# Kernel tuning notes

Measured on AMD Instinct MI355X. Metric: run time of the kernel, lower is better.

The kernel has to match this reference:

```python
import jax, jax.numpy as jnp
import numpy as np

G = 16       # groups
GRID = 25    # hardcoded self.grid
EPS = 1e-5   # BatchNorm eps


def _gconv(x, w, pad):
    # x: (B, Cin, H, W), w: (Cout, Cin//G, kh, kw); grouped conv, stride 1
    return jax.lax.conv_general_dilated(
        x, w, window_strides=(1, 1), padding=[(pad, pad), (pad, pad)],
        feature_group_count=G)


def _bn_relu(h, g, b, m, v):
    # h: (G, B, C, H, W); per-group-instance BN params: (G, C). Inference BN.
    scale = (g / jnp.sqrt(v + EPS))[:, None, :, None, None]
    return jax.nn.relu((h - m[:, None, :, None, None]) * scale + b[:, None, :, None, None])


def setup_inputs() -> dict:
    key = jax.random.key(0)
    ks = jax.random.split(key, 11)
    B, C, H, W = 2, 256, 24, 24
    AC = GRID * C  # 6400 affinity channels
    return {
        "x":  jax.random.normal(ks[0], (B, C, H, W), jnp.float32),
        "W1": jax.random.normal(ks[1], (G, C, C // G, 3, 3), jnp.float32) * 0.05,
        "g1": jax.random.uniform(ks[2], (G, C), jnp.float32, 0.5, 1.5),
        "b1": jax.random.normal(ks[3], (G, C), jnp.float32) * 0.1,
        "m1": jax.random.normal(ks[4], (G, C), jnp.float32) * 0.1,
        "v1": jax.random.uniform(ks[5], (G, C), jnp.float32, 0.5, 1.5),
        "W2": jax.random.normal(ks[6], (G, AC, C // G, 1, 1), jnp.float32) * 0.05,
        "g2": jax.random.uniform(ks[7], (G, AC), jnp.float32, 0.5, 1.5),
        "b2": jax.random.normal(ks[8], (G, AC), jnp.float32) * 0.1,
        "m2": jax.random.normal(ks[9], (G, AC), jnp.float32) * 0.1,
        "v2": jax.random.uniform(ks[10], (G, AC), jnp.float32, 0.5, 1.5),
    }


def reference(x, W1, g1, b1, m1, v1, W2, g2, b2, m2, v2):
    B, C, H, W = x.shape
    Cg = C // G
    # 16 independent grouped 3x3 convs over the same input, batched via vmap
    h1 = jax.vmap(lambda w: _gconv(x, w, 1))(W1)          # (G, B, C, H, W)
    h1 = _bn_relu(h1, g1, b1, m1, v1)
    # grouped 1x1 conv with padding=1 (faithful to source -> spatial grows to H+2, W+2)
    a = jax.vmap(lambda h, w: _gconv(h, w, 1))(h1, W2)    # (G, B, 25C, H+2, W+2)
    a = _bn_relu(a, g2, b2, m2, v2)
    pooled = a.mean(axis=(-2, -1))                        # adaptive avg pool -> (G, B, 25C)
    xv = pooled.reshape(G, B, G, GRID * Cg)               # (G, B, G, 25*Cg)
    aff = jnp.einsum('ibkm,iblm->ibkl', xv, xv)           # (G, B, G, G) = theta @ phi
    idx = jnp.arange(G)
    aff_i = aff[idx, :, idx, :] / G                       # aff[:, i], /N  -> (G, B, G)
    ex = h1.reshape(G, B, G, Cg * H * W)
    # torch.matmul((B,G), (B,G,M)) broadcasts 2-D lhs -> (B, B, M); kept faithfully
    z = jnp.einsum('ipk,iqkm->ipqm', aff_i, ex)           # (G, B, B, Cg*H*W)
    z = z.reshape(G, B, B, Cg, H, W).transpose(1, 0, 2, 3, 4, 5)
    return z.reshape(B, G * B * Cg, H, W)                 # (B, B*C, H, W)
```

## Files before the change

kernel.cpp:

```cpp
#include <hip/hip_runtime.h>
#include <hip/hip_bf16.h>


typedef __attribute__((ext_vector_type(8))) short short8;
typedef __attribute__((ext_vector_type(4))) float f32x4;

static __device__ __forceinline__ unsigned short f2bf(float x) {
    unsigned u = __float_as_uint(x);
    unsigned r = (u + 0x7fffu + ((u >> 16) & 1u)) >> 16;
    return (unsigned short)r;
}

#define WA_OFF   33696
#define WLB_OFF  23040
#define B2_OFF   35840
#define PACC_OFF 37440
#define ZP_OFF   39040
#define BB1_OFF  40096
#define SMEM_BYTES 40160

__global__ __launch_bounds__(512, 4) void k12_fused(
    const float* __restrict__ xin,
    const float* __restrict__ W1,
    const float* __restrict__ g1, const float* __restrict__ b1,
    const float* __restrict__ m1, const float* __restrict__ v1,
    const float* __restrict__ W2,
    const float* __restrict__ g2, const float* __restrict__ b2,
    const float* __restrict__ m2, const float* __restrict__ v2,
    unsigned short* __restrict__ h1b,
    float* __restrict__ pooled)
{
    __shared__ __align__(16) char smem[SMEM_BYTES];
    short* xs    = (short*)smem;
    short* wAp   = (short*)(smem + WA_OFF);
    short* hsb   = (short*)smem;
    short* wlb   = (short*)(smem + WLB_OFF);
    float* bias2 = (float*)(smem + B2_OFF);
    float* pacc  = (float*)(smem + PACC_OFF);
    float* bias1 = (float*)(smem + BB1_OFF);

    int bid = blockIdx.x;
    int i = bid >> 5, b = (bid >> 4) & 1, g = bid & 15;
    int t = threadIdx.x;

    float4 w2r[4];
    float  bsc;
    {
        bool act = (t < 400);
        int o = i*6400 + g*400 + (act ? t : 0);
        float s2 = g2[o] * rsqrtf(v2[o] + 1e-5f);
        bsc = b2[o] - m2[o] * s2;
        const float4* wr = (const float4*)&W2[o*16];
#pragma unroll
        for (int q = 0; q < 4; q++) {
            float4 wv = wr[q];
            wv.x *= s2; wv.y *= s2; wv.z *= s2; wv.w *= s2;
            w2r[q] = wv;
        }
    }

    if (t < 16) {
        int c = i*256 + g*16 + t;
        float sc = g1[c] * rsqrtf(v1[c] + 1e-5f);
        bias1[t] = b1[c] - m1[c] * sc;
    }
    {
        int* xz = (int*)xs;
        for (int idx = t; idx < 1512; idx += 512) {
            int c = idx / 12, j = idx - (idx / 12) * 12;
            int row, col;
            if (c < 26)      { row = 0;  col = c; }
            else if (c < 52) { row = 25; col = c - 26; }
            else if (c < 78) { row = 26; col = c - 52; }
            else { int k = c - 78; row = 1 + (k >> 1); col = (k & 1) ? 25 : 0; }
            xz[(row*26 + col)*12 + j] = 0;
        }
    }
    {
        const float* xb = &xin[(b*256 + g*16)*576];
        for (int idx = t; idx < 9216; idx += 512) {
            int ci = idx / 576; int s = idx - ci*576;
            int y = s / 24; int x = s - y*24;
            xs[((y+1)*26 + (x+1))*24 + ci] = (short)f2bf(xb[idx]);
        }
    }
    {
        const float* wb = &W1[(i*256 + g*16)*144];
        for (int idx = t; idx < 2560; idx += 512) {
            int kk = idx >> 9, rem = idx & 511, co = rem >> 5, k = rem & 31;
            int tap = 2*kk + (k >> 4), ci = k & 15;
            int c = i*256 + g*16 + co;
            float sc = g1[c] * rsqrtf(v1[c] + 1e-5f);
            float val = (tap < 9) ? wb[co*144 + ci*9 + tap] * sc : 0.f;
            wAp[(kk*16 + co)*40 + k] = (short)f2bf(val);
        }
    }
    __syncthreads();

    int l = t & 63, w = t >> 6;
    int quad = l >> 4, rc = l & 15;
    bool five = (w < 4);

    f32x4 dreg[5];
    {
        int ci0 = (quad & 1) * 8;
        short8 afr[5];
#pragma unroll
        for (int kk = 0; kk < 5; kk++)
            afr[kk] = *(const short8*)&wAp[(kk*16 + rc)*40 + quad*8];
        f32x4 cb1 = *(const f32x4*)&bias1[quad*4];

        const int offE[5] = {0, 48, 648, 1248, 1296};
        const int offO[5] = {24, 624, 672, 1272, 1872};
        int off[5];
#pragma unroll
        for (int kk = 0; kk < 5; kk++) off[kk] = (quad >= 2) ? offO[kk] : offE[kk];

#pragma unroll
        for (int tt = 0; tt < 5; tt++) {
            if (tt == 4 && !five) break;
            int s = (tt*8 + w)*16 + rc;
            int y = s / 24; int x = s - y*24;
            int base = (y*26 + x)*24 + ci0;
            f32x4 acc = cb1;
#pragma unroll
            for (int kk = 0; kk < 5; kk++) {
                short8 bf = *(const short8*)&xs[base + off[kk]];
                acc = __builtin_amdgcn_mfma_f32_16x16x32_bf16(afr[kk], bf, acc, 0, 0, 0);
            }
#pragma unroll
            for (int r = 0; r < 4; r++) acc[r] = fmaxf(acc[r], 0.f);
            dreg[tt] = acc;
        }
    }
    __syncthreads();

    {
        unsigned short* hout = &h1b[((i*2 + b)*256 + g*16)*576];
#pragma unroll
        for (int tt = 0; tt < 5; tt++) {
            if (tt == 4 && !five) break;
            int s = (tt*8 + w)*16 + rc;
            f32x4 acc = dreg[tt];
            unsigned short e0 = f2bf(acc[0]), e1 = f2bf(acc[1]);
            unsigned short e2 = f2bf(acc[2]), e3 = f2bf(acc[3]);
            uint2 pk = {(unsigned)e0 | ((unsigned)e1 << 16),
                        (unsigned)e2 | ((unsigned)e3 << 16)};
            *(uint2*)&hsb[s*20 + quad*4] = pk;
            hout[(quad*4 + 0)*576 + s] = e0;
            hout[(quad*4 + 1)*576 + s] = e1;
            hout[(quad*4 + 2)*576 + s] = e2;
            hout[(quad*4 + 3)*576 + s] = e3;
        }
    }
    if (t < 400) {
        pacc[t]  = 0.f;
        bias2[t] = bsc;
#pragma unroll
        for (int q = 0; q < 4; q++) {
            float4 wv = w2r[q];
            wlb[t*16 + q*4 + 0] = (short)f2bf(wv.x);
            wlb[t*16 + q*4 + 1] = (short)f2bf(wv.y);
            wlb[t*16 + q*4 + 2] = (short)f2bf(wv.z);
            wlb[t*16 + q*4 + 3] = (short)f2bf(wv.w);
        }
    }
    if (t < 4) ((int*)(smem + ZP_OFF))[t] = 0;
    __syncthreads();

    {
        int q8 = (quad & 1) * 8;
        short8 af2[5];
#pragma unroll
        for (int u = 0; u < 5; u++) {
            bool valid = (l < 32) && (u < 4 || five);
            int boff = valid ? ((((u*8 + w)*16 + rc)*20 + q8)*2) : ZP_OFF;
            af2[u] = *(const short8*)(smem + boff);
        }
        for (int mt = 0; mt < 25; mt++) {
            int m0 = mt*16;
            int woff = (l < 32) ? (WLB_OFF + ((m0 + rc)*16 + q8)*2) : ZP_OFF;
            short8 wf = *(const short8*)(smem + woff);
            float be = bias2[m0 + rc];
            f32x4 cb = {be, be, be, be};

            f32x4 accv = {0.f, 0.f, 0.f, 0.f};
#pragma unroll
            for (int u = 0; u < 4; u++) {
                f32x4 d = __builtin_amdgcn_mfma_f32_16x16x32_bf16(af2[u], wf, cb, 0, 0, 0);
#pragma unroll
                for (int r = 0; r < 4; r++)
                    accv[r] += fmaxf(d[r], 0.f);
            }
            if (five) {
                f32x4 d = __builtin_amdgcn_mfma_f32_16x16x32_bf16(af2[4], wf, cb, 0, 0, 0);
#pragma unroll
                for (int r = 0; r < 4; r++)
                    accv[r] += fmaxf(d[r], 0.f);
            }
            float a = (accv[0] + accv[1]) + (accv[2] + accv[3]);
            a += __shfl_xor(a, 16);
            a += __shfl_xor(a, 32);
            if (l < 16)
                atomicAdd(&pacc[m0 + l], a);
        }
    }
    __syncthreads();

    const float inv = 1.f / 676.f;
    if (t < 400) {
        float be = bias2[t];
        pooled[(i*2+b)*6400 + g*400 + t] =
            (pacc[t] + 100.f * fmaxf(be, 0.f)) * inv;
    }
}

__global__ __launch_bounds__(256) void k3_aff(const float* __restrict__ pooled,
                                              float* __restrict__ aff)
{
    __shared__ float th[400];
    __shared__ float parts[256];
    int bid = blockIdx.x;
    int i = bid >> 1;
    int t = threadIdx.x;
    const float* pb = &pooled[bid*6400];
    for (int idx = t; idx < 400; idx += 256) th[idx] = pb[i*400 + idx];
    __syncthreads();
    int l = t >> 4, p = t & 15;
    float sum = 0.f;
    const float* pl = &pb[l*400];
    for (int m = p*25; m < p*25 + 25; m++) sum = fmaf(th[m], pl[m], sum);
    parts[t] = sum;
    __syncthreads();
    if (t < 16) {
        float s = 0.f;
        for (int pp = 0; pp < 16; pp++) s += parts[t*16 + pp];
        aff[bid*16 + t] = s * (1.f/16.f);
    }
}

__global__ __launch_bounds__(256) void k4_out(const unsigned short* __restrict__ h1b,
                                              const float* __restrict__ aff,
                                              float* __restrict__ out)
{
    __shared__ float a0[16], a1[16];
    int bid = blockIdx.x;
    int i = bid >> 5, q = (bid >> 4) & 1, cg = bid & 15;
    int t = threadIdx.x;
    if (t < 16) a0[t] = aff[(i*2+0)*16 + t];
    else if (t < 32) a1[t-16] = aff[(i*2+1)*16 + (t-16)];
    __syncthreads();
    if (t >= 144) return;
    const unsigned short* hb = &h1b[((i*2+q)*256 + cg)*576];
    int ch = i*32 + q*16 + cg;
    int s = t*4;
    float c00=0.f,c01=0.f,c02=0.f,c03=0.f;
    float c10=0.f,c11=0.f,c12=0.f,c13=0.f;
#pragma unroll
    for (int k = 0; k < 16; k++) {
        uint2 hv = *(const uint2*)&hb[k*9216 + s];
        float p0 = __uint_as_float(hv.x << 16);
        float p1 = __uint_as_float(hv.x & 0xffff0000u);
        float p2 = __uint_as_float(hv.y << 16);
        float p3 = __uint_as_float(hv.y & 0xffff0000u);
        float va = a0[k], vb = a1[k];
        c00 = fmaf(va, p0, c00); c01 = fmaf(va, p1, c01);
        c02 = fmaf(va, p2, c02); c03 = fmaf(va, p3, c03);
        c10 = fmaf(vb, p0, c10); c11 = fmaf(vb, p1, c11);
        c12 = fmaf(vb, p2, c12); c13 = fmaf(vb, p3, c13);
    }
    float4 o0 = {c00, c01, c02, c03};
    float4 o1 = {c10, c11, c12, c13};
    *(float4*)&out[ch*576 + s]         = o0;
    *(float4*)&out[(512 + ch)*576 + s] = o1;
}

extern "C" void kernel_launch(void* const* d_in, const int* in_sizes, int n_in,
                              void* d_out, int out_size, void* d_ws, size_t ws_size,
                              hipStream_t stream)
{
    const float* x  = (const float*)d_in[0];
    const float* W1 = (const float*)d_in[1];
    const float* g1 = (const float*)d_in[2];
    const float* b1 = (const float*)d_in[3];
    const float* m1 = (const float*)d_in[4];
    const float* v1 = (const float*)d_in[5];
    const float* W2 = (const float*)d_in[6];
    const float* g2 = (const float*)d_in[7];
    const float* b2 = (const float*)d_in[8];
    const float* m2 = (const float*)d_in[9];
    const float* v2 = (const float*)d_in[10];

    unsigned short* h1b = (unsigned short*)d_ws;
    float* pooled = (float*)(h1b + 16*2*256*576);
    float* aff    = pooled + 204800;

    float* out = (float*)d_out;

    hipLaunchKernelGGL(k12_fused, dim3(512), dim3(512), 0, stream,
                       x, W1, g1, b1, m1, v1, W2, g2, b2, m2, v2, h1b, pooled);
    hipLaunchKernelGGL(k3_aff,    dim3(32),  dim3(256), 0, stream,
                       pooled, aff);
    hipLaunchKernelGGL(k4_out,    dim3(512), dim3(256), 0, stream,
                       h1b, aff, out);
}
```

Baseline: 111.1 us.

## Fuse affinity reduction into output kernel and vectorize input staging loads

Removes the separate k3_aff launch. Each k4_out block now recomputes the 32 affinity values it needs straight from the pooled features, using 8-lane float2 dot products and a shuffle reduction. Separately, the input staging in k12_fused now reads float4 and writes four transposed bf16 values per thread. This saves one kernel launch and its serialization gap, at the cost of recomputing the affinity dot products redundantly in every one of the 512 output blocks.

```diff
diff --git a/kernel.cpp b/kernel.cpp
--- a/kernel.cpp
+++ b/kernel.cpp
@@ -77,11 +77,17 @@
         }
     }
     {
-        const float* xb = &xin[(b*256 + g*16)*576];
-        for (int idx = t; idx < 9216; idx += 512) {
-            int ci = idx / 576; int s = idx - ci*576;
+        const float4* xb4 = (const float4*)&xin[(b*256 + g*16)*576];
+        for (int idx = t; idx < 2304; idx += 512) {
+            float4 v = xb4[idx];
+            int f = idx * 4;
+            int ci = f / 576; int s = f - ci*576;
             int y = s / 24; int x = s - y*24;
-            xs[((y+1)*26 + (x+1))*24 + ci] = (short)f2bf(xb[idx]);
+            int base = ((y+1)*26 + (x+1))*24 + ci;
+            xs[base     ] = (short)f2bf(v.x);
+            xs[base + 24] = (short)f2bf(v.y);
+            xs[base + 48] = (short)f2bf(v.z);
+            xs[base + 72] = (short)f2bf(v.w);
         }
     }
     {
@@ -215,41 +221,38 @@
     }
 }
 
-__global__ __launch_bounds__(256) void k3_aff(const float* __restrict__ pooled,
-                                              float* __restrict__ aff)
-{
-    __shared__ float th[400];
-    __shared__ float parts[256];
-    int bid = blockIdx.x;
-    int i = bid >> 1;
-    int t = threadIdx.x;
-    const float* pb = &pooled[bid*6400];
-    for (int idx = t; idx < 400; idx += 256) th[idx] = pb[i*400 + idx];
-    __syncthreads();
-    int l = t >> 4, p = t & 15;
-    float sum = 0.f;
-    const float* pl = &pb[l*400];
-    for (int m = p*25; m < p*25 + 25; m++) sum = fmaf(th[m], pl[m], sum);
-    parts[t] = sum;
-    __syncthreads();
-    if (t < 16) {
-        float s = 0.f;
-        for (int pp = 0; pp < 16; pp++) s += parts[t*16 + pp];
-        aff[bid*16 + t] = s * (1.f/16.f);
-    }
-}
-
 __global__ __launch_bounds__(256) void k4_out(const unsigned short* __restrict__ h1b,
-                                              const float* __restrict__ aff,
+                                              const float* __restrict__ pooled,
                                               float* __restrict__ out)
 {
     __shared__ float a0[16], a1[16];
     int bid = blockIdx.x;
     int i = bid >> 5, q = (bid >> 4) & 1, cg = bid & 15;
     int t = threadIdx.x;
-    if (t < 16) a0[t] = aff[(i*2+0)*16 + t];
-    else if (t < 32) a1[t-16] = aff[(i*2+1)*16 + (t-16)];
-    __syncthreads();
+
+    {
+        int p = t >> 3, j = t & 7;
+        int bb = p >> 4, l = p & 15;
+        const float* pb = &pooled[(i*2 + bb)*6400];
+        const float2* pth = (const float2*)(pb + i*400);
+        const float2* pl  = (const float2*)(pb + l*400);
+        float s = 0.f;
+#pragma unroll 5
+        for (int f = j; f < 200; f += 8) {
+            float2 a = pth[f], c = pl[f];
+            s = fmaf(a.x, c.x, s);
+            s = fmaf(a.y, c.y, s);
+        }
+        s += __shfl_xor(s, 1);
+        s += __shfl_xor(s, 2);
+        s += __shfl_xor(s, 4);
+        if (j == 0) {
+            float v = s * (1.f/16.f);
+            if (bb == 0) a0[l] = v; else a1[l] = v;
+        }
+    }
+    __syncthreads();
+
     if (t >= 144) return;
     const unsigned short* hb = &h1b[((i*2+q)*256 + cg)*576];
     int ch = i*32 + q*16 + cg;
@@ -293,14 +296,11 @@
 
     unsigned short* h1b = (unsigned short*)d_ws;
     float* pooled = (float*)(h1b + 16*2*256*576);
-    float* aff    = pooled + 204800;
 
     float* out = (float*)d_out;
 
     hipLaunchKernelGGL(k12_fused, dim3(512), dim3(512), 0, stream,
                        x, W1, g1, b1, m1, v1, W2, g2, b2, m2, v2, h1b, pooled);
-    hipLaunchKernelGGL(k3_aff,    dim3(32),  dim3(256), 0, stream,
-                       pooled, aff);
     hipLaunchKernelGGL(k4_out,    dim3(512), dim3(256), 0, stream,
-                       h1b, aff, out);
+                       h1b, pooled, out);
 }
```

Measured after the change: 111.7 us. About the same (+0.6%).
